# Kernel tuning notes

Measured on AMD Instinct MI355X. Metric: run time of the kernel, lower is better.

The kernel has to match this reference:

```python
import jax, jax.numpy as jnp
import numpy as np

N = 100000   # nodes
E = 1600000  # edges (avg degree 16)
F = 128      # num_features
H = 128      # hidden
BN_EPS = 1e-5
NORM_EPS = 1e-12


def setup_inputs() -> dict:
    key = jax.random.key(0)
    k = jax.random.split(key, 5)
    x = jax.random.normal(k[0], (N, F), dtype=jnp.float32)
    edge_index = jax.random.randint(k[1], (2, E), 0, N, dtype=jnp.int64)
    # Xavier-uniform linear weights (as in weights_init)
    s = float(np.sqrt(6.0 / (F + H)))
    W_l = jax.random.uniform(k[2], (F, H), jnp.float32, -s, s)  # neighbor branch
    b_l = jnp.zeros((H,), jnp.float32)
    W_r = jax.random.uniform(k[3], (F, H), jnp.float32, -s, s)  # root branch (no bias in PyG)
    gamma = jnp.ones((H,), jnp.float32)   # BatchNorm weight
    beta = jnp.zeros((H,), jnp.float32)   # BatchNorm bias
    return {"x": x, "edge_index": edge_index, "W_l": W_l, "b_l": b_l,
            "W_r": W_r, "gamma": gamma, "beta": beta}


def reference(x, edge_index, W_l, b_l, W_r, gamma, beta):
    n = x.shape[0]
    src, dst = edge_index[0], edge_index[1]
    # mean aggregation of neighbor messages x_j at destination nodes
    agg = jax.ops.segment_sum(x[src], dst, num_segments=n)                 # [N, F]
    deg = jax.ops.segment_sum(jnp.ones((src.shape[0],), x.dtype), dst,
                              num_segments=n)                              # [N]
    agg = agg / jnp.maximum(deg, 1.0)[:, None]
    # SAGEConv: lin_l(agg) + lin_r(x), then row-wise L2 normalize
    out = agg @ W_l + b_l + x @ W_r                                        # [N, H]
    nrm = jnp.sqrt(jnp.sum(out * out, axis=-1, keepdims=True))
    out = out / jnp.maximum(nrm, NORM_EPS)
    # transition: ReLU -> BatchNorm1d (batch stats, training mode) -> Dropout(identity)
    out = jax.nn.relu(out)
    mean = jnp.mean(out, axis=0)
    var = jnp.mean((out - mean) ** 2, axis=0)  # biased variance (torch BN)
    out = (out - mean) / jnp.sqrt(var + BN_EPS) * gamma + beta
    return out
```

## Files before the change

kernel.cpp:

```cpp
#include <hip/hip_runtime.h>
#include <hip/hip_bf16.h>

static constexpr int F = 128;
static constexpr int H = 128;
static constexpr int NPART = 128;

typedef __attribute__((ext_vector_type(8))) short short8;
typedef __attribute__((ext_vector_type(4))) float f32x4;
typedef __attribute__((ext_vector_type(2))) _Float16 h2v;

__device__ __forceinline__ unsigned short f2bf(float f) {
  union { float f; unsigned u; } a; a.f = f;
  unsigned r = a.u + 0x7FFF + ((a.u >> 16) & 1);
  return (unsigned short)(r >> 16);
}
__device__ __forceinline__ float bf2f(unsigned short h) {
  union { unsigned u; float f; } a; a.u = ((unsigned)h) << 16;
  return a.f;
}
__device__ __forceinline__ float bits2f(unsigned u) {
  union { unsigned u; float f; } a; a.u = u;
  return a.f;
}
__device__ __forceinline__ h2v bits2h2(unsigned u) {
  union { unsigned u; h2v h; } a; a.u = u; return a.h;
}

__device__ __forceinline__ unsigned f2fp8(float f) {
  union { float f; unsigned u; } a; a.f = f;
  unsigned s = (a.u >> 24) & 0x80u;
  unsigned m = a.u & 0x7FFFFFFFu;
  if (m < 0x3C800000u) return s;
  unsigned r = m + 0x7FFFFu + ((m >> 20) & 1u);
  if (r > 0x43E00000u) r = 0x43E00000u;
  return s | ((((r >> 23) - 120u) & 15u) << 3) | ((r >> 20) & 7u);
}

__device__ __forceinline__ void fp8x4_to_h2(unsigned w, h2v& p02, h2v& p13) {
  unsigned lo = w & 0x00FF00FFu;
  unsigned hi = (w >> 8) & 0x00FF00FFu;
  unsigned q0 = (((lo << 7) & 0x3F803F80u) + 0x20002000u) | ((lo & 0x00800080u) << 8);
  unsigned q1 = (((hi << 7) & 0x3F803F80u) + 0x20002000u) | ((hi & 0x00800080u) << 8);
  p02 = bits2h2(q0);
  p13 = bits2h2(q1);
}

__device__ __forceinline__ void fp8x4_to_f32(unsigned w, float& f0, float& f1,
                                             float& f2, float& f3) {
  unsigned lo = w & 0x00FF00FFu;
  unsigned hi = (w >> 8) & 0x00FF00FFu;
  unsigned p0 = (((lo << 4) & 0x07F007F0u) + 0x3C003C00u) | ((lo & 0x00800080u) << 8);
  unsigned p1 = (((hi << 4) & 0x07F007F0u) + 0x3C003C00u) | ((hi & 0x00800080u) << 8);
  f0 = bits2f(p0 << 16);
  f2 = bits2f(p0 & 0xFFFF0000u);
  f1 = bits2f(p1 << 16);
  f3 = bits2f(p1 & 0xFFFF0000u);
}

__device__ __forceinline__ int detect64(const void* eiv) {
  const unsigned* u = (const unsigned*)eiv;
  int is64 = 1;
  for (int i = 0; i < 64; ++i) is64 &= (u[2 * i + 1] == 0u);
  return is64;
}

__global__ void detect_dtype(const unsigned* __restrict__ ei, int* __restrict__ flag) {
  if (blockIdx.x == 0 && threadIdx.x == 0) {
    int is64 = 1;
    for (int i = 0; i < 64; ++i) {
      if (ei[2 * i + 1] != 0u) { is64 = 0; break; }
    }
    *flag = is64;
  }
}

__device__ __forceinline__ int load_idx(const void* eiv, int is64, long long pos) {
  return is64 ? (int)((const long long*)eiv)[pos] : ((const int*)eiv)[pos];
}

__global__ __launch_bounds__(256) void scan1(const int* __restrict__ in,
                                             int* __restrict__ outx,
                                             int* __restrict__ blocksum, int n) {
  __shared__ int sm[256];
  int idx = blockIdx.x * 256 + threadIdx.x;
  int v = (idx < n) ? in[idx] : 0;
  sm[threadIdx.x] = v;
  __syncthreads();
  #pragma unroll
  for (int off = 1; off < 256; off <<= 1) {
    int t = (threadIdx.x >= off) ? sm[threadIdx.x - off] : 0;
    __syncthreads();
    sm[threadIdx.x] += t;
    __syncthreads();
  }
  if (idx < n) outx[idx] = sm[threadIdx.x] - v;
  if (threadIdx.x == 255) blocksum[blockIdx.x] = sm[255];
}

__global__ __launch_bounds__(1024) void scan2big(const int* __restrict__ blocksum,
                                                 int* __restrict__ blockoff, int nb) {
  __shared__ int sm[1024];
  int t = threadIdx.x;
  int v = (t < nb) ? blocksum[t] : 0;
  sm[t] = v;
  __syncthreads();
  for (int off = 1; off < 1024; off <<= 1) {
    int u = (t >= off) ? sm[t - off] : 0;
    __syncthreads();
    sm[t] += u;
    __syncthreads();
  }
  if (t < nb) blockoff[t] = sm[t] - v;
}

__global__ __launch_bounds__(256) void scan3p(int* __restrict__ obuf,
                                              const int* __restrict__ blockoff,
                                              int* __restrict__ bbase,
                                              float* __restrict__ colzero,
                                              int L, int nbuck, int E) {
  if (blockIdx.x == 0) colzero[threadIdx.x] = 0.0f;
  int idx = blockIdx.x * 256 + threadIdx.x;
  if (idx >= L) return;
  int v = obuf[idx] + blockoff[idx >> 8];
  obuf[idx] = v;
  if ((idx & (NPART - 1)) == 0) bbase[idx / NPART] = v;
  if (idx == 0) bbase[nbuck] = E;
}

__global__ __launch_bounds__(512) void part_scatter(const void* __restrict__ eiv,
                                                    const int* __restrict__ base,
                                                    int* __restrict__ ebuf,
                                                    int E, int nbuck, int chunk) {
  __shared__ int cur[2048];
  const int t = threadIdx.x, b = blockIdx.x;
  for (int i = t; i < nbuck; i += 512) cur[i] = base[i * NPART + b];
  __syncthreads();
  int is64 = detect64(eiv);
  int s = b * chunk, e = min(E, s + chunk);
  for (int i = s + t; i < e; i += 512) {
    int src = load_idx(eiv, is64, i);
    int dst = load_idx(eiv, is64, (long long)E + i);
    int pos = atomicAdd(&cur[dst >> 6], 1);
    ebuf[pos] = (src << 6) | (dst & 63);
  }
}

__global__ __launch_bounds__(256) void prep_w(const float* __restrict__ Wl,
                                              const float* __restrict__ Wr,
                                              unsigned short* __restrict__ Wcat) {
  int tid = blockIdx.x * 256 + threadIdx.x;
  if (tid >= 4 * 4 * 8 * 64) return;
  int lane = tid & 63;
  int nf   = (tid >> 6) & 7;
  int kc   = (tid >> 9) & 3;
  int part = tid >> 11;
  const float* W = (part < 2) ? Wl : Wr;
  bool lo = (part & 1);
  int ncol = nf * 16 + (lane & 15);
  int k0 = kc * 32 + (lane >> 4) * 8;
  unsigned short ov[8];
  #pragma unroll
  for (int j = 0; j < 8; ++j) {
    float v = W[(k0 + j) * H + ncol];
    unsigned short h = f2bf(v);
    ov[j] = lo ? f2bf(v - bf2f(h)) : h;
  }
  uint4 pack;
  pack.x = (unsigned)ov[0] | ((unsigned)ov[1] << 16);
  pack.y = (unsigned)ov[2] | ((unsigned)ov[3] << 16);
  pack.z = (unsigned)ov[4] | ((unsigned)ov[5] << 16);
  pack.w = (unsigned)ov[6] | ((unsigned)ov[7] << 16);
  *(uint4*)(Wcat + (size_t)tid * 8) = pack;
}

template <bool LOWP>
__global__ __launch_bounds__(256) void fused_gemm_hist(
    const float* __restrict__ x, const unsigned short* __restrict__ Wcat,
    const float* __restrict__ bl, unsigned char* __restrict__ Yf8,
    float* __restrict__ pout, unsigned short* __restrict__ Pbf, int n,
    const void* __restrict__ eiv, int* __restrict__ cmat, int E, int nbuck,
    int chunk) {
  __shared__ unsigned short As[2][64][128];

  const int t = threadIdx.x;

  if (blockIdx.x < NPART) {
    int* h = (int*)&As[0][0][0];
    const int b = blockIdx.x;
    for (int i = t; i < nbuck; i += 256) h[i] = 0;
    __syncthreads();
    int is64 = detect64(eiv);
    int s = b * chunk, e = min(E, s + chunk);
    for (int i = s + t; i < e; i += 256) {
      int dst = load_idx(eiv, is64, (long long)E + i);
      atomicAdd(&h[dst >> 6], 1);
    }
    __syncthreads();
    for (int i = t; i < nbuck; i += 256) cmat[i * NPART + b] = h[i];
    return;
  }

  const int i0 = (blockIdx.x - NPART) * 64;

  #pragma unroll
  for (int it = 0; it < 8; ++it) {
    int idx = it * 256 + t;
    int r = idx >> 5;
    int c4 = (idx & 31) * 4;
    int row_g = i0 + r; if (row_g >= n) row_g = n - 1;
    int boff = (((c4 >> 3) ^ (r & 7)) << 3) + (c4 & 7);
    float4 vx = *(const float4*)(x + (size_t)row_g * F + c4);
    unsigned short h0 = f2bf(vx.x), h1 = f2bf(vx.y), h2 = f2bf(vx.z), h3 = f2bf(vx.w);
    uint2 hv = { (unsigned)h0 | ((unsigned)h1 << 16), (unsigned)h2 | ((unsigned)h3 << 16) };
    *(uint2*)&As[0][r][boff] = hv;
    unsigned short l0 = f2bf(vx.x - bf2f(h0)), l1 = f2bf(vx.y - bf2f(h1));
    unsigned short l2 = f2bf(vx.z - bf2f(h2)), l3 = f2bf(vx.w - bf2f(h3));
    uint2 lv = { (unsigned)l0 | ((unsigned)l1 << 16), (unsigned)l2 | ((unsigned)l3 << 16) };
    *(uint2*)&As[1][r][boff] = lv;
  }
  __syncthreads();

  const int w = t >> 6;
  const int lane = t & 63;

  f32x4 accL[4][2], accR[4][2];
  #pragma unroll
  for (int rf = 0; rf < 4; ++rf)
    #pragma unroll
    for (int nfi = 0; nfi < 2; ++nfi) {
      accL[rf][nfi] = (f32x4){0.f, 0.f, 0.f, 0.f};
      accR[rf][nfi] = (f32x4){0.f, 0.f, 0.f, 0.f};
    }

  const int APM[3] = {0, 1, 0};
  const int BL[3]  = {0, 0, 1};
  const int BR[3]  = {2, 2, 3};

  #pragma unroll
  for (int pass = 0; pass < 3; ++pass) {
    const int ap = APM[pass];
    #pragma unroll
    for (int kc = 0; kc < 4; ++kc) {
      short8 afr[4];
      int chunk2 = kc * 4 + (lane >> 4);
      #pragma unroll
      for (int rf = 0; rf < 4; ++rf) {
        int row = rf * 16 + (lane & 15);
        afr[rf] = *(const short8*)(&As[ap][row][(chunk2 ^ (row & 7)) * 8]);
      }
      short8 bfrL[2], bfrR[2];
      #pragma unroll
      for (int nfi = 0; nfi < 2; ++nfi) {
        int blobL = (BL[pass] * 4 + kc) * 8 + (w * 2 + nfi);
        int blobR = (BR[pass] * 4 + kc) * 8 + (w * 2 + nfi);
        bfrL[nfi] = *(const short8*)(Wcat + (size_t)blobL * 512 + lane * 8);
        bfrR[nfi] = *(const short8*)(Wcat + (size_t)blobR * 512 + lane * 8);
      }
      #pragma unroll
      for (int rf = 0; rf < 4; ++rf)
        #pragma unroll
        for (int nfi = 0; nfi < 2; ++nfi) {
          accL[rf][nfi] = __builtin_amdgcn_mfma_f32_16x16x32_bf16(
              afr[rf], bfrL[nfi], accL[rf][nfi], 0, 0, 0);
          accR[rf][nfi] = __builtin_amdgcn_mfma_f32_16x16x32_bf16(
              afr[rf], bfrR[nfi], accR[rf][nfi], 0, 0, 0);
        }
    }
  }

  const float b0 = bl[w * 32 + (lane & 15)];
  const float b1 = bl[w * 32 + 16 + (lane & 15)];

  #pragma unroll
  for (int rf = 0; rf < 4; ++rf) {
    #pragma unroll
    for (int r4 = 0; r4 < 4; ++r4) {
      int rl = rf * 16 + (lane >> 4) * 4 + r4;
      int row = i0 + rl;
      if (row < n) {
        Yf8[(size_t)row * H + w * 32 + (lane & 15)]      = (unsigned char)f2fp8(accL[rf][0][r4]);
        Yf8[(size_t)row * H + w * 32 + 16 + (lane & 15)] = (unsigned char)f2fp8(accL[rf][1][r4]);
        if (LOWP) {
          Pbf[(size_t)row * H + w * 32 + (lane & 15)]      = f2bf(accR[rf][0][r4] + b0);
          Pbf[(size_t)row * H + w * 32 + 16 + (lane & 15)] = f2bf(accR[rf][1][r4] + b1);
        } else {
          pout[(size_t)row * H + w * 32 + (lane & 15)]      = accR[rf][0][r4] + b0;
          pout[(size_t)row * H + w * 32 + 16 + (lane & 15)] = accR[rf][1][r4] + b1;
        }
      }
    }
  }
}

#define GCAP 2048
template <bool LOWP>
__global__ __launch_bounds__(256) void gather_bucket(
    const unsigned char* __restrict__ Yf8, const int* __restrict__ ebuf,
    const int* __restrict__ bbase, float* __restrict__ pio,
    const unsigned short* __restrict__ Pbf, unsigned short* __restrict__ Ubf,
    float* __restrict__ colsum, float* __restrict__ colsq, int n) {
  __shared__ int lsrc[GCAP];
  __shared__ int hist[65];
  __shared__ int loff[65];
  __shared__ int cur[64];
  __shared__ float csm[128], cqm[128];

  const int t = threadIdx.x;
  const int b = blockIdx.x;
  const int node0 = b << 6;
  const int s = bbase[b], e = bbase[b + 1];
  const int cnt = e - s;

  if (t < 65) hist[t] = 0;
  if (t < 128) { csm[t] = 0.f; cqm[t] = 0.f; }
  __syncthreads();

  const bool fast = (cnt <= GCAP);
  if (fast) {
    for (int i = s + t; i < e; i += 256)
      atomicAdd(&hist[ebuf[i] & 63], 1);
    __syncthreads();
    if (t < 64) loff[t] = hist[t];
    __syncthreads();
    #pragma unroll
    for (int off = 1; off < 64; off <<= 1) {
      int u = (t >= off && t < 64) ? loff[t - off] : 0;
      __syncthreads();
      if (t < 64) loff[t] += u;
      __syncthreads();
    }
    if (t < 64) cur[t] = loff[t] - hist[t];
    __syncthreads();
    for (int i = s + t; i < e; i += 256) {
      int p = ebuf[i];
      int pos = atomicAdd(&cur[p & 63], 1);
      lsrc[pos] = p >> 6;
    }
    __syncthreads();
  }

  const int lane = t & 63;
  const int w = t >> 6;
  const int half = lane >> 5;
  const int c = (lane & 31) * 4;

  float lcs[4] = {0.f, 0.f, 0.f, 0.f};
  float lcq[4] = {0.f, 0.f, 0.f, 0.f};

  #pragma unroll
  for (int it = 0; it < 8; ++it) {
    int ln = it * 8 + w * 2 + half;
    int node = node0 + ln;
    if (node >= n) continue;
    int ls, le;
    if (fast) { ls = loff[ln] - hist[ln]; le = loff[ln]; }
    else      { ls = 0; le = 0; }

    h2v a02[8], a13[8];
    #pragma unroll
    for (int u = 0; u < 8; ++u) {
      a02[u] = (h2v)(_Float16)0;
      a13[u] = (h2v)(_Float16)0;
    }

    int j = ls;
    for (; j + 7 < le; j += 8) {
      #pragma unroll
      for (int u = 0; u < 8; ++u) {
        int sj = lsrc[j + u];
        unsigned wv = *(const unsigned*)(Yf8 + (size_t)sj * H + c);
        h2v p02, p13;
        fp8x4_to_h2(wv, p02, p13);
        a02[u] += p02;
        a13[u] += p13;
      }
    }
    for (; j + 1 < le; j += 2) {
      #pragma unroll
      for (int u = 0; u < 2; ++u) {
        int sj = lsrc[j + u];
        unsigned wv = *(const unsigned*)(Yf8 + (size_t)sj * H + c);
        h2v p02, p13;
        fp8x4_to_h2(wv, p02, p13);
        a02[u] += p02;
        a13[u] += p13;
      }
    }
    if (j < le) {
      int sj = lsrc[j];
      unsigned wv = *(const unsigned*)(Yf8 + (size_t)sj * H + c);
      h2v p02, p13;
      fp8x4_to_h2(wv, p02, p13);
      a02[0] += p02;
      a13[0] += p13;
    }

    float deg = 0.0f;
    float a0, a1, a2, a3;
    if (fast) {
      deg = (float)(le - ls);
      h2v s02 = ((a02[0] + a02[1]) + (a02[2] + a02[3])) +
                ((a02[4] + a02[5]) + (a02[6] + a02[7]));
      h2v s13 = ((a13[0] + a13[1]) + (a13[2] + a13[3])) +
                ((a13[4] + a13[5]) + (a13[6] + a13[7]));
      a0 = (float)s02[0]; a2 = (float)s02[1];
      a1 = (float)s13[0]; a3 = (float)s13[1];
    } else {
      a0 = a1 = a2 = a3 = 0.0f;
      for (int jj = s; jj < e; ++jj) {
        int p = ebuf[jj];
        if ((p & 63) == ln) {
          deg += 1.0f;
          unsigned wv = *(const unsigned*)(Yf8 + (size_t)(p >> 6) * H + c);
          float f0, f1, f2, f3;
          fp8x4_to_f32(wv, f0, f1, f2, f3);
          a0 += f0; a1 += f1; a2 += f2; a3 += f3;
        }
      }
    }

    float inv = 1.0f / fmaxf(deg, 1.0f);
    float p0, p1, p2, p3;
    if (LOWP) {
      uint2 pv = *(const uint2*)(Pbf + (size_t)node * H + c);
      p0 = bits2f(pv.x << 16);
      p1 = bits2f(pv.x & 0xFFFF0000u);
      p2 = bits2f(pv.y << 16);
      p3 = bits2f(pv.y & 0xFFFF0000u);
    } else {
      float4 p = *(const float4*)(pio + (size_t)node * H + c);
      p0 = p.x; p1 = p.y; p2 = p.z; p3 = p.w;
    }
    float v0 = p0 + a0 * inv;
    float v1 = p1 + a1 * inv;
    float v2 = p2 + a2 * inv;
    float v3 = p3 + a3 * inv;
    float sq = v0 * v0 + v1 * v1 + v2 * v2 + v3 * v3;
    sq += __shfl_xor(sq, 1, 64);
    sq += __shfl_xor(sq, 2, 64);
    sq += __shfl_xor(sq, 4, 64);
    sq += __shfl_xor(sq, 8, 64);
    sq += __shfl_xor(sq, 16, 64);
    float rs = 1.0f / fmaxf(sqrtf(sq), 1e-12f);
    float u0 = fmaxf(v0 * rs, 0.f), u1 = fmaxf(v1 * rs, 0.f);
    float u2 = fmaxf(v2 * rs, 0.f), u3 = fmaxf(v3 * rs, 0.f);
    if (LOWP) {
      uint2 ov;
      ov.x = (unsigned)f2bf(u0) | ((unsigned)f2bf(u1) << 16);
      ov.y = (unsigned)f2bf(u2) | ((unsigned)f2bf(u3) << 16);
      *(uint2*)(Ubf + (size_t)node * H + c) = ov;
    } else {
      float4 o = {u0, u1, u2, u3};
      *(float4*)(pio + (size_t)node * H + c) = o;
    }
    lcs[0] += u0; lcq[0] += u0 * u0;
    lcs[1] += u1; lcq[1] += u1 * u1;
    lcs[2] += u2; lcq[2] += u2 * u2;
    lcs[3] += u3; lcq[3] += u3 * u3;
  }

  #pragma unroll
  for (int q = 0; q < 4; ++q) {
    atomicAdd(&csm[c + q], lcs[q]);
    atomicAdd(&cqm[c + q], lcq[q]);
  }
  __syncthreads();
  if (t < 128) {
    atomicAdd(&colsum[t], csm[t]);
    atomicAdd(&colsq[t], cqm[t]);
  }
}

__global__ __launch_bounds__(256) void deg_count(const void* __restrict__ eiv,
                                                 const int* __restrict__ flag,
                                                 int* __restrict__ degi, int E) {
  int e = blockIdx.x * blockDim.x + threadIdx.x;
  if (e >= E) return;
  int dst = load_idx(eiv, *flag, (long long)E + e);
  atomicAdd(&degi[dst], 1);
}

__global__ __launch_bounds__(256) void scan3(int* __restrict__ offsets,
                                             const int* __restrict__ blockoff,
                                             int* __restrict__ cursor, int n, int E) {
  int idx = blockIdx.x * 256 + threadIdx.x;
  if (idx >= n) return;
  int off = offsets[idx] + blockoff[idx >> 8];
  offsets[idx] = off;
  cursor[idx] = off;
  if (idx == 0) offsets[n] = E;
}

__global__ __launch_bounds__(256) void bucket_fill(const void* __restrict__ eiv,
                                                   const int* __restrict__ flag,
                                                   int* __restrict__ cursor,
                                                   int* __restrict__ csr_src, int E) {
  int e = blockIdx.x * blockDim.x + threadIdx.x;
  if (e >= E) return;
  int is64 = *flag;
  int src = load_idx(eiv, is64, e);
  int dst = load_idx(eiv, is64, (long long)E + e);
  int pos = atomicAdd(&cursor[dst], 1);
  csr_src[pos] = src;
}

__global__ __launch_bounds__(256) void gather_mean(const float* __restrict__ x,
                                                   const int* __restrict__ offsets,
                                                   const int* __restrict__ csr_src,
                                                   float* __restrict__ out, int n) {
  int node = (int)(((long long)blockIdx.x * blockDim.x + threadIdx.x) >> 6);
  int lane = threadIdx.x & 63;
  if (node >= n) return;
  int s = offsets[node], e = offsets[node + 1];
  float ax = 0.0f, ay = 0.0f, bx = 0.0f, by = 0.0f;
  int j = s;
  for (; j + 1 < e; j += 2) {
    int s0 = csr_src[j], s1 = csr_src[j + 1];
    float2 v0 = *(const float2*)(x + (size_t)s0 * F + lane * 2);
    float2 v1 = *(const float2*)(x + (size_t)s1 * F + lane * 2);
    ax += v0.x; ay += v0.y;
    bx += v1.x; by += v1.y;
  }
  if (j < e) {
    int s0 = csr_src[j];
    float2 v0 = *(const float2*)(x + (size_t)s0 * F + lane * 2);
    ax += v0.x; ay += v0.y;
  }
  float inv = 1.0f / fmaxf((float)(e - s), 1.0f);
  float2 r; r.x = (ax + bx) * inv; r.y = (ay + by) * inv;
  *(float2*)(out + (size_t)node * H + lane * 2) = r;
}

__global__ __launch_bounds__(256) void mfma_gemm(
    const float* __restrict__ x, const unsigned short* __restrict__ Wcat,
    const float* __restrict__ bl, float* __restrict__ out,
    float* __restrict__ colsum, float* __restrict__ colsq, int n) {
  __shared__ unsigned short As[4][64][128];
  __shared__ float rowsq[64][4];
  __shared__ float rscale[64];

  const int t = threadIdx.x;
  const int i0 = blockIdx.x * 64;

  #pragma unroll
  for (int it = 0; it < 8; ++it) {
    int idx = it * 256 + t;
    int r = idx >> 5;
    int c4 = (idx & 31) * 4;
    int row_g = i0 + r; if (row_g >= n) row_g = n - 1;
    int boff = (((c4 >> 3) ^ (r & 7)) << 3) + (c4 & 7);
    float4 va = *(const float4*)(out + (size_t)row_g * H + c4);
    float4 vx = *(const float4*)(x + (size_t)row_g * H + c4);
    unsigned short h0 = f2bf(va.x), h1 = f2bf(va.y), h2 = f2bf(va.z), h3 = f2bf(va.w);
    uint2 hv = { (unsigned)h0 | ((unsigned)h1 << 16), (unsigned)h2 | ((unsigned)h3 << 16) };
    *(uint2*)&As[0][r][boff] = hv;
    unsigned short l0 = f2bf(va.x - bf2f(h0)), l1 = f2bf(va.y - bf2f(h1));
    unsigned short l2 = f2bf(va.z - bf2f(h2)), l3 = f2bf(va.w - bf2f(h3));
    uint2 lv = { (unsigned)l0 | ((unsigned)l1 << 16), (unsigned)l2 | ((unsigned)l3 << 16) };
    *(uint2*)&As[1][r][boff] = lv;
    h0 = f2bf(vx.x); h1 = f2bf(vx.y); h2 = f2bf(vx.z); h3 = f2bf(vx.w);
    uint2 hx = { (unsigned)h0 | ((unsigned)h1 << 16), (unsigned)h2 | ((unsigned)h3 << 16) };
    *(uint2*)&As[2][r][boff] = hx;
    l0 = f2bf(vx.x - bf2f(h0)); l1 = f2bf(vx.y - bf2f(h1));
    l2 = f2bf(vx.z - bf2f(h2)); l3 = f2bf(vx.w - bf2f(h3));
    uint2 lx = { (unsigned)l0 | ((unsigned)l1 << 16), (unsigned)l2 | ((unsigned)l3 << 16) };
    *(uint2*)&As[3][r][boff] = lx;
  }
  __syncthreads();

  const int w = t >> 6;
  const int lane = t & 63;

  f32x4 acc[4][2];
  #pragma unroll
  for (int rf = 0; rf < 4; ++rf)
    #pragma unroll
    for (int nfi = 0; nfi < 2; ++nfi)
      acc[rf][nfi] = (f32x4){0.f, 0.f, 0.f, 0.f};

  const int APM[6] = {0, 1, 0, 2, 3, 2};
  const int BPM[6] = {0, 0, 1, 2, 2, 3};

  #pragma unroll
  for (int pass = 0; pass < 6; ++pass) {
    const int ap = APM[pass], bp = BPM[pass];
    #pragma unroll
    for (int kc = 0; kc < 4; ++kc) {
      short8 bfr[2];
      #pragma unroll
      for (int nfi = 0; nfi < 2; ++nfi) {
        int blob = (bp * 4 + kc) * 8 + (w * 2 + nfi);
        bfr[nfi] = *(const short8*)(Wcat + (size_t)blob * 512 + lane * 8);
      }
      short8 afr[4];
      int chunk = kc * 4 + (lane >> 4);
      #pragma unroll
      for (int rf = 0; rf < 4; ++rf) {
        int row = rf * 16 + (lane & 15);
        afr[rf] = *(const short8*)(&As[ap][row][(chunk ^ (row & 7)) * 8]);
      }
      #pragma unroll
      for (int rf = 0; rf < 4; ++rf)
        #pragma unroll
        for (int nfi = 0; nfi < 2; ++nfi)
          acc[rf][nfi] = __builtin_amdgcn_mfma_f32_16x16x32_bf16(
              afr[rf], bfr[nfi], acc[rf][nfi], 0, 0, 0);
    }
  }

  const float b0 = bl[w * 32 + (lane & 15)];
  const float b1 = bl[w * 32 + 16 + (lane & 15)];

  #pragma unroll
  for (int rf = 0; rf < 4; ++rf) {
    #pragma unroll
    for (int r4 = 0; r4 < 4; ++r4) {
      float v0 = acc[rf][0][r4] + b0;
      float v1 = acc[rf][1][r4] + b1;
      acc[rf][0][r4] = v0;
      acc[rf][1][r4] = v1;
      float sq = v0 * v0 + v1 * v1;
      sq += __shfl_xor(sq, 1, 64);
      sq += __shfl_xor(sq, 2, 64);
      sq += __shfl_xor(sq, 4, 64);
      sq += __shfl_xor(sq, 8, 64);
      if ((lane & 15) == 0) rowsq[rf * 16 + (lane >> 4) * 4 + r4][w] = sq;
    }
  }
  __syncthreads();
  if (t < 64) {
    float s = rowsq[t][0] + rowsq[t][1] + rowsq[t][2] + rowsq[t][3];
    rscale[t] = 1.0f / fmaxf(sqrtf(s), 1e-12f);
  }
  __syncthreads();

  float cs0 = 0.f, cq0 = 0.f, cs1 = 0.f, cq1 = 0.f;
  #pragma unroll
  for (int rf = 0; rf < 4; ++rf) {
    #pragma unroll
    for (int r4 = 0; r4 < 4; ++r4) {
      int rl = rf * 16 + (lane >> 4) * 4 + r4;
      int row = i0 + rl;
      float s = rscale[rl];
      float u0 = fmaxf(acc[rf][0][r4] * s, 0.f);
      float u1 = fmaxf(acc[rf][1][r4] * s, 0.f);
      if (row < n) {
        out[(size_t)row * H + w * 32 + (lane & 15)] = u0;
        out[(size_t)row * H + w * 32 + 16 + (lane & 15)] = u1;
        cs0 += u0; cq0 += u0 * u0;
        cs1 += u1; cq1 += u1 * u1;
      }
    }
  }
  cs0 += __shfl_xor(cs0, 16, 64); cs0 += __shfl_xor(cs0, 32, 64);
  cq0 += __shfl_xor(cq0, 16, 64); cq0 += __shfl_xor(cq0, 32, 64);
  cs1 += __shfl_xor(cs1, 16, 64); cs1 += __shfl_xor(cs1, 32, 64);
  cq1 += __shfl_xor(cq1, 16, 64); cq1 += __shfl_xor(cq1, 32, 64);
  if (lane < 16) {
    atomicAdd(&colsum[w * 32 + lane], cs0);
    atomicAdd(&colsq[w * 32 + lane], cq0);
    atomicAdd(&colsum[w * 32 + 16 + lane], cs1);
    atomicAdd(&colsq[w * 32 + 16 + lane], cq1);
  }
}

__global__ __launch_bounds__(256) void scatter_mean(
    const float* __restrict__ x, const void* __restrict__ eiv,
    const int* __restrict__ flag, float* __restrict__ agg,
    float* __restrict__ deg, int E) {
  long long gid = (long long)blockIdx.x * blockDim.x + threadIdx.x;
  int e = (int)(gid >> 5);
  int ch = (int)(gid & 31);
  if (e >= E) return;
  int is64 = *flag;
  int src = load_idx(eiv, is64, e);
  int dst = load_idx(eiv, is64, (long long)E + e);
  float4 v = *(const float4*)(x + (size_t)src * F + ch * 4);
  float* a = agg + (size_t)dst * H + ch * 4;
  atomicAdd(a + 0, v.x);
  atomicAdd(a + 1, v.y);
  atomicAdd(a + 2, v.z);
  atomicAdd(a + 3, v.w);
  if (ch == 0) atomicAdd(deg + dst, 1.0f);
}

__global__ __launch_bounds__(256) void divide_deg(float* __restrict__ out,
                                                  const float* __restrict__ deg,
                                                  long long n4) {
  long long i = (long long)blockIdx.x * blockDim.x + threadIdx.x;
  if (i >= n4) return;
  int node = (int)(i >> 5);
  float s = 1.0f / fmaxf(deg[node], 1.0f);
  float4 v = ((float4*)out)[i];
  v.x *= s; v.y *= s; v.z *= s; v.w *= s;
  ((float4*)out)[i] = v;
}

__global__ __launch_bounds__(256) void fused_gemm(
    const float* __restrict__ x, const float* __restrict__ Wl,
    const float* __restrict__ bl, const float* __restrict__ Wr,
    float* __restrict__ out, float* __restrict__ colsum, float* __restrict__ colsq) {
  __shared__ float As[16][256];
  __shared__ float rp[4][8];
  __shared__ float rscale[16];
  __shared__ float cs[128], cs2[128];

  const int t = threadIdx.x;
  const int i0 = blockIdx.x * 16;

  #pragma unroll
  for (int it = 0; it < 2; ++it) {
    int idx = (it * 256 + t) * 4;
    int r = idx >> 7, c = idx & 127;
    float4 va = *(const float4*)(out + (size_t)(i0 + r) * H + c);
    As[r][c + 0] = va.x; As[r][c + 1] = va.y;
    As[r][c + 2] = va.z; As[r][c + 3] = va.w;
    float4 vx = *(const float4*)(x + (size_t)(i0 + r) * F + c);
    As[r][128 + c + 0] = vx.x; As[r][128 + c + 1] = vx.y;
    As[r][128 + c + 2] = vx.z; As[r][128 + c + 3] = vx.w;
  }
  __syncthreads();

  const int c = t & 127;
  const int half = t >> 7;
  float acc[8];
  #pragma unroll
  for (int r = 0; r < 8; ++r) acc[r] = 0.0f;

  #pragma unroll 4
  for (int k = 0; k < 128; ++k) {
    float w = Wl[k * H + c];
    #pragma unroll
    for (int r = 0; r < 8; ++r) acc[r] = fmaf(As[half * 8 + r][k], w, acc[r]);
  }
  #pragma unroll 4
  for (int k = 0; k < 128; ++k) {
    float w = Wr[k * H + c];
    #pragma unroll
    for (int r = 0; r < 8; ++r) acc[r] = fmaf(As[half * 8 + r][128 + k], w, acc[r]);
  }
  const float bias = bl[c];
  #pragma unroll
  for (int r = 0; r < 8; ++r) acc[r] += bias;

  float sq[8];
  #pragma unroll
  for (int r = 0; r < 8; ++r) sq[r] = acc[r] * acc[r];
  #pragma unroll
  for (int off = 32; off > 0; off >>= 1) {
    #pragma unroll
    for (int r = 0; r < 8; ++r) sq[r] += __shfl_down(sq[r], off, 64);
  }
  const int wv = t >> 6;
  if ((t & 63) == 0) {
    #pragma unroll
    for (int r = 0; r < 8; ++r) rp[wv][r] = sq[r];
  }
  __syncthreads();
  if (t < 16) {
    int base = (t >> 3) * 2, rr = t & 7;
    float s = rp[base][rr] + rp[base + 1][rr];
    rscale[t] = 1.0f / fmaxf(sqrtf(s), 1e-12f);
  }
  __syncthreads();

  float csum = 0.0f, csq = 0.0f;
  #pragma unroll
  for (int r = 0; r < 8; ++r) {
    float v = fmaxf(acc[r] * rscale[half * 8 + r], 0.0f);
    out[(size_t)(i0 + half * 8 + r) * H + c] = v;
    csum += v;
    csq += v * v;
  }
  if (half == 1) { cs[c] = csum; cs2[c] = csq; }
  __syncthreads();
  if (half == 0) {
    atomicAdd(&colsum[c], csum + cs[c]);
    atomicAdd(&colsq[c], csq + cs2[c]);
  }
}

__global__ void bn_stats(const float* __restrict__ colsum, const float* __restrict__ colsq,
                         const float* __restrict__ gamma, const float* __restrict__ beta,
                         float* __restrict__ scale, float* __restrict__ shift, int n) {
  int c = threadIdx.x;
  if (c < H) {
    float inv_n = 1.0f / (float)n;
    float mean = colsum[c] * inv_n;
    float var = colsq[c] * inv_n - mean * mean;
    float istd = rsqrtf(var + 1e-5f);
    float sc = gamma[c] * istd;
    scale[c] = sc;
    shift[c] = beta[c] - mean * sc;
  }
}

__global__ __launch_bounds__(256) void bn_apply(
    float* __restrict__ out, const float* __restrict__ scale,
    const float* __restrict__ shift, long long n4) {
  long long i = (long long)blockIdx.x * blockDim.x + threadIdx.x;
  if (i >= n4) return;
  float4 v = ((float4*)out)[i];
  int c = (int)((i * 4) & (H - 1));
  v.x = fmaf(v.x, scale[c + 0], shift[c + 0]);
  v.y = fmaf(v.y, scale[c + 1], shift[c + 1]);
  v.z = fmaf(v.z, scale[c + 2], shift[c + 2]);
  v.w = fmaf(v.w, scale[c + 3], shift[c + 3]);
  ((float4*)out)[i] = v;
}

__global__ __launch_bounds__(256) void bn_apply_lo(
    const unsigned short* __restrict__ U, float* __restrict__ out,
    const float* __restrict__ scale, const float* __restrict__ shift,
    long long n4) {
  long long i = (long long)blockIdx.x * blockDim.x + threadIdx.x;
  if (i >= n4) return;
  uint2 uv = ((const uint2*)U)[i];
  int c = (int)((i * 4) & (H - 1));
  float4 v;
  v.x = fmaf(bits2f(uv.x << 16),          scale[c + 0], shift[c + 0]);
  v.y = fmaf(bits2f(uv.x & 0xFFFF0000u),  scale[c + 1], shift[c + 1]);
  v.z = fmaf(bits2f(uv.y << 16),          scale[c + 2], shift[c + 2]);
  v.w = fmaf(bits2f(uv.y & 0xFFFF0000u),  scale[c + 3], shift[c + 3]);
  ((float4*)out)[i] = v;
}

extern "C" void kernel_launch(void* const* d_in, const int* in_sizes, int n_in,
                              void* d_out, int out_size, void* d_ws, size_t ws_size,
                              hipStream_t stream) {
  const float* x     = (const float*)d_in[0];
  const void*  ei    = d_in[1];
  const float* Wl    = (const float*)d_in[2];
  const float* bl    = (const float*)d_in[3];
  const float* Wr    = (const float*)d_in[4];
  const float* gamma = (const float*)d_in[5];
  const float* beta  = (const float*)d_in[6];
  float* out = (float*)d_out;

  const int n = in_sizes[0] / F;
  const int E = in_sizes[1] / 2;
  const int nb = (n + 255) / 256;
  const int nbuck = (n + 63) >> 6;

  char* ws = (char*)d_ws;
  int* flag = (int*)ws;
  unsigned short* Wcat = (unsigned short*)(ws + 256);
  char* after_w = ws + 256 + 4 * 128 * 128 * 2;

  int*   cmat    = (int*)after_w;
  int*   obuf    = cmat + 2048 * NPART;
  int*   bsum    = obuf + 2048 * NPART;
  int*   boff    = bsum + 1024;
  int*   bbase   = boff + 1024;
  float* fcs     = (float*)(bbase + 2049);
  float* fcq     = fcs + H;
  float* fsc     = fcq + H;
  float* fsh     = fsc + H;
  int*   ebuf    = (int*)(fsh + H);
  unsigned char*  Yf8 = (unsigned char*)(ebuf + E);
  unsigned short* Pws = (unsigned short*)(Yf8 + (size_t)n * H);
  unsigned short* Uws = Pws + (size_t)n * H;
  size_t need_fast  = (size_t)((char*)(Yf8 + (size_t)n * H) - ws);
  size_t need_fast2 = (size_t)((char*)(Uws + (size_t)n * H) - ws);

  int*   degi     = (int*)after_w;
  int*   offsets  = degi + n;
  int*   cursor   = offsets + n + 1;
  int*   blocksum = cursor + n;
  int*   blockoff = blocksum + nb;
  float* mcs      = (float*)(blockoff + nb);
  float* mcq      = mcs + H;
  float* msc      = mcq + H;
  float* msh      = msc + H;
  int*   csr_src  = (int*)(msh + H);
  size_t need_mid = (size_t)((char*)(csr_src + E) - ws);

  float *colsum, *colsq, *scale, *shift;

  const int eb = (E + 255) / 256;
  const int gb = (n + 63) / 64;
  const long long n4 = (long long)n * H / 4;

  if (ws_size >= need_fast && nbuck <= 2048) {
    const bool lowp = (ws_size >= need_fast2);
    colsum = fcs; colsq = fcq; scale = fsc; shift = fsh;

    const int chunk = (E + NPART - 1) / NPART;
    const int L = nbuck * NPART;
    const int nb2 = (L + 255) / 256;

    prep_w<<<32, 256, 0, stream>>>(Wl, Wr, Wcat);
    if (lowp)
      fused_gemm_hist<true><<<NPART + gb, 256, 0, stream>>>(
          x, Wcat, bl, Yf8, out, Pws, n, ei, cmat, E, nbuck, chunk);
    else
      fused_gemm_hist<false><<<NPART + gb, 256, 0, stream>>>(
          x, Wcat, bl, Yf8, out, Pws, n, ei, cmat, E, nbuck, chunk);

    scan1<<<nb2, 256, 0, stream>>>(cmat, obuf, bsum, L);
    scan2big<<<1, 1024, 0, stream>>>(bsum, boff, nb2);
    scan3p<<<nb2, 256, 0, stream>>>(obuf, boff, bbase, colsum, L, nbuck, E);
    part_scatter<<<NPART, 512, 0, stream>>>(ei, obuf, ebuf, E, nbuck, chunk);

    if (lowp)
      gather_bucket<true><<<nbuck, 256, 0, stream>>>(
          Yf8, ebuf, bbase, out, Pws, Uws, colsum, colsq, n);
    else
      gather_bucket<false><<<nbuck, 256, 0, stream>>>(
          Yf8, ebuf, bbase, out, Pws, Uws, colsum, colsq, n);

    bn_stats<<<1, 128, 0, stream>>>(colsum, colsq, gamma, beta, scale, shift, n);
    if (lowp)
      bn_apply_lo<<<(int)((n4 + 255) / 256), 256, 0, stream>>>(
          Uws, out, scale, shift, n4);
    else
      bn_apply<<<(int)((n4 + 255) / 256), 256, 0, stream>>>(out, scale, shift, n4);
  } else if (ws_size >= need_mid) {
    colsum = mcs; colsq = mcq; scale = msc; shift = msh;
    detect_dtype<<<1, 64, 0, stream>>>((const unsigned*)ei, flag);
    hipMemsetAsync(degi, 0, (size_t)n * 4, stream);
    hipMemsetAsync(colsum, 0, 2 * H * 4, stream);

    prep_w<<<32, 256, 0, stream>>>(Wl, Wr, Wcat);

    deg_count<<<eb, 256, 0, stream>>>(ei, flag, degi, E);
    scan1<<<nb, 256, 0, stream>>>(degi, offsets, blocksum, n);
    scan2big<<<1, 1024, 0, stream>>>(blocksum, blockoff, nb);
    scan3<<<nb, 256, 0, stream>>>(offsets, blockoff, cursor, n, E);
    bucket_fill<<<eb, 256, 0, stream>>>(ei, flag, cursor, csr_src, E);

    long long gthreads = (long long)n * 64;
    gather_mean<<<(int)((gthreads + 255) / 256), 256, 0, stream>>>(
        x, offsets, csr_src, out, n);

    mfma_gemm<<<gb, 256, 0, stream>>>(x, Wcat, bl, out, colsum, colsq, n);
    bn_stats<<<1, 128, 0, stream>>>(colsum, colsq, gamma, beta, scale, shift, n);
    bn_apply<<<(int)((n4 + 255) / 256), 256, 0, stream>>>(out, scale, shift, n4);
  } else {
    float* deg = (float*)(ws + 256);
    colsum = deg + n; colsq = colsum + H; scale = colsq + H; shift = scale + H;
    detect_dtype<<<1, 64, 0, stream>>>((const unsigned*)ei, flag);
    hipMemsetAsync(d_out, 0, (size_t)out_size * sizeof(float), stream);
    hipMemsetAsync(deg, 0, (size_t)n * 4 + 4 * H * 4, stream);
    long long sthreads = (long long)E * 32;
    scatter_mean<<<(int)((sthreads + 255) / 256), 256, 0, stream>>>(x, ei, flag, out, deg, E);
    long long n4f = (long long)n * H / 4;
    divide_deg<<<(int)((n4f + 255) / 256), 256, 0, stream>>>(out, deg, n4f);
    fused_gemm<<<n / 16, 256, 0, stream>>>(x, Wl, bl, Wr, out, colsum, colsq);
    bn_stats<<<1, 128, 0, stream>>>(colsum, colsq, gamma, beta, scale, shift, n);
    bn_apply<<<(int)((n4 + 255) / 256), 256, 0, stream>>>(out, scale, shift, n4);
  }
}
```

Measured before the change: 190.6 us.

## Regroup kernels: fuse histogram with weight prep, scatter with GEMM

Moves the per-partition edge histogram out of the GEMM kernel into a new kernel launched together with the weight-packing blocks. The edge scatter-by-bucket now runs inside the GEMM kernel in place of the histogram. The GEMM overlaps with the heavier scatter pass instead of the light histogram, and one launch is removed. The cost is that the GEMM can no longer start until the scans finish, and the scatter blocks now use 256 threads instead of 512.

```diff
diff --git a/kernel.cpp b/kernel.cpp
--- a/kernel.cpp
+++ b/kernel.cpp
@@ -127,28 +127,29 @@
   if (idx == 0) bbase[nbuck] = E;
 }
 
-__global__ __launch_bounds__(512) void part_scatter(const void* __restrict__ eiv,
-                                                    const int* __restrict__ base,
-                                                    int* __restrict__ ebuf,
-                                                    int E, int nbuck, int chunk) {
-  __shared__ int cur[2048];
-  const int t = threadIdx.x, b = blockIdx.x;
-  for (int i = t; i < nbuck; i += 512) cur[i] = base[i * NPART + b];
-  __syncthreads();
-  int is64 = detect64(eiv);
-  int s = b * chunk, e = min(E, s + chunk);
-  for (int i = s + t; i < e; i += 512) {
-    int src = load_idx(eiv, is64, i);
-    int dst = load_idx(eiv, is64, (long long)E + i);
-    int pos = atomicAdd(&cur[dst >> 6], 1);
-    ebuf[pos] = (src << 6) | (dst & 63);
-  }
-}
-
-__global__ __launch_bounds__(256) void prep_w(const float* __restrict__ Wl,
-                                              const float* __restrict__ Wr,
-                                              unsigned short* __restrict__ Wcat) {
-  int tid = blockIdx.x * 256 + threadIdx.x;
+__global__ __launch_bounds__(256) void union_hist_prep(
+    const void* __restrict__ eiv, int* __restrict__ cmat, int E, int nbuck,
+    int chunk, const float* __restrict__ Wl, const float* __restrict__ Wr,
+    unsigned short* __restrict__ Wcat) {
+  __shared__ int h[2048];
+  const int t = threadIdx.x;
+
+  if (blockIdx.x < NPART) {
+    const int b = blockIdx.x;
+    for (int i = t; i < nbuck; i += 256) h[i] = 0;
+    __syncthreads();
+    int is64 = detect64(eiv);
+    int s = b * chunk, e = min(E, s + chunk);
+    for (int i = s + t; i < e; i += 256) {
+      int dst = load_idx(eiv, is64, (long long)E + i);
+      atomicAdd(&h[dst >> 6], 1);
+    }
+    __syncthreads();
+    for (int i = t; i < nbuck; i += 256) cmat[i * NPART + b] = h[i];
+    return;
+  }
+
+  int tid = (blockIdx.x - NPART) * 256 + t;
   if (tid >= 4 * 4 * 8 * 64) return;
   int lane = tid & 63;
   int nf   = (tid >> 6) & 7;
@@ -162,8 +163,8 @@
   #pragma unroll
   for (int j = 0; j < 8; ++j) {
     float v = W[(k0 + j) * H + ncol];
-    unsigned short h = f2bf(v);
-    ov[j] = lo ? f2bf(v - bf2f(h)) : h;
+    unsigned short hh = f2bf(v);
+    ov[j] = lo ? f2bf(v - bf2f(hh)) : hh;
   }
   uint4 pack;
   pack.x = (unsigned)ov[0] | ((unsigned)ov[1] << 16);
@@ -174,29 +175,29 @@
 }
 
 template <bool LOWP>
-__global__ __launch_bounds__(256) void fused_gemm_hist(
+__global__ __launch_bounds__(256) void union_scatter_gemm(
+    const void* __restrict__ eiv, const int* __restrict__ base,
+    int* __restrict__ ebuf, int E, int nbuck, int chunk,
     const float* __restrict__ x, const unsigned short* __restrict__ Wcat,
     const float* __restrict__ bl, unsigned char* __restrict__ Yf8,
-    float* __restrict__ pout, unsigned short* __restrict__ Pbf, int n,
-    const void* __restrict__ eiv, int* __restrict__ cmat, int E, int nbuck,
-    int chunk) {
+    float* __restrict__ pout, unsigned short* __restrict__ Pbf, int n) {
   __shared__ unsigned short As[2][64][128];
 
   const int t = threadIdx.x;
 
   if (blockIdx.x < NPART) {
-    int* h = (int*)&As[0][0][0];
+    int* cur = (int*)&As[0][0][0];
     const int b = blockIdx.x;
-    for (int i = t; i < nbuck; i += 256) h[i] = 0;
+    for (int i = t; i < nbuck; i += 256) cur[i] = base[i * NPART + b];
     __syncthreads();
     int is64 = detect64(eiv);
     int s = b * chunk, e = min(E, s + chunk);
     for (int i = s + t; i < e; i += 256) {
+      int src = load_idx(eiv, is64, i);
       int dst = load_idx(eiv, is64, (long long)E + i);
-      atomicAdd(&h[dst >> 6], 1);
-    }
-    __syncthreads();
-    for (int i = t; i < nbuck; i += 256) cmat[i * NPART + b] = h[i];
+      int pos = atomicAdd(&cur[dst >> 6], 1);
+      ebuf[pos] = (src << 6) | (dst & 63);
+    }
     return;
   }
 
@@ -504,6 +505,34 @@
   csr_src[pos] = src;
 }
 
+__global__ __launch_bounds__(256) void prep_w(const float* __restrict__ Wl,
+                                              const float* __restrict__ Wr,
+                                              unsigned short* __restrict__ Wcat) {
+  int tid = blockIdx.x * 256 + threadIdx.x;
+  if (tid >= 4 * 4 * 8 * 64) return;
+  int lane = tid & 63;
+  int nf   = (tid >> 6) & 7;
+  int kc   = (tid >> 9) & 3;
+  int part = tid >> 11;
+  const float* W = (part < 2) ? Wl : Wr;
+  bool lo = (part & 1);
+  int ncol = nf * 16 + (lane & 15);
+  int k0 = kc * 32 + (lane >> 4) * 8;
+  unsigned short ov[8];
+  #pragma unroll
+  for (int j = 0; j < 8; ++j) {
+    float v = W[(k0 + j) * H + ncol];
+    unsigned short h = f2bf(v);
+    ov[j] = lo ? f2bf(v - bf2f(h)) : h;
+  }
+  uint4 pack;
+  pack.x = (unsigned)ov[0] | ((unsigned)ov[1] << 16);
+  pack.y = (unsigned)ov[2] | ((unsigned)ov[3] << 16);
+  pack.z = (unsigned)ov[4] | ((unsigned)ov[5] << 16);
+  pack.w = (unsigned)ov[6] | ((unsigned)ov[7] << 16);
+  *(uint4*)(Wcat + (size_t)tid * 8) = pack;
+}
+
 __global__ __launch_bounds__(256) void gather_mean(const float* __restrict__ x,
                                                    const int* __restrict__ offsets,
                                                    const int* __restrict__ csr_src,
@@ -889,18 +918,19 @@
     const int L = nbuck * NPART;
     const int nb2 = (L + 255) / 256;
 
-    prep_w<<<32, 256, 0, stream>>>(Wl, Wr, Wcat);
-    if (lowp)
-      fused_gemm_hist<true><<<NPART + gb, 256, 0, stream>>>(
-          x, Wcat, bl, Yf8, out, Pws, n, ei, cmat, E, nbuck, chunk);
-    else
-      fused_gemm_hist<false><<<NPART + gb, 256, 0, stream>>>(
-          x, Wcat, bl, Yf8, out, Pws, n, ei, cmat, E, nbuck, chunk);
+    union_hist_prep<<<NPART + 32, 256, 0, stream>>>(
+        ei, cmat, E, nbuck, chunk, Wl, Wr, Wcat);
 
     scan1<<<nb2, 256, 0, stream>>>(cmat, obuf, bsum, L);
     scan2big<<<1, 1024, 0, stream>>>(bsum, boff, nb2);
     scan3p<<<nb2, 256, 0, stream>>>(obuf, boff, bbase, colsum, L, nbuck, E);
-    part_scatter<<<NPART, 512, 0, stream>>>(ei, obuf, ebuf, E, nbuck, chunk);
+
+    if (lowp)
+      union_scatter_gemm<true><<<NPART + gb, 256, 0, stream>>>(
+          ei, obuf, ebuf, E, nbuck, chunk, x, Wcat, bl, Yf8, out, Pws, n);
+    else
+      union_scatter_gemm<false><<<NPART + gb, 256, 0, stream>>>(
+          ei, obuf, ebuf, E, nbuck, chunk, x, Wcat, bl, Yf8, out, Pws, n);
 
     if (lowp)
       gather_bucket<true><<<nbuck, 256, 0, stream>>>(
```

After: 188.8 us. Within noise of the previous version (-0.9%).
